# Performance work log

Measured on AMD Instinct MI355X. Metric: run time of the kernel, lower is better.

## Reference

```python
import jax, jax.numpy as jnp
import numpy as np

DIM = 256
HEADS = 8
HEAD_DIM = DIM // HEADS
SCALE = HEAD_DIM ** -0.5
WD, WH, WW = 2, 7, 7
N = WD * WH * WW            # 98 tokens per window
NW = 256                    # windows per sample
B = 2048                    # batch * num_windows
PBT_LEN = (2 * WD - 1) * (2 * WH - 1) * (2 * WW - 1)  # 507


def _relative_position_index():
    # Deterministic buffer from __init__: [N, N] int indices into pbt rows.
    coords = np.stack(np.meshgrid(np.arange(WD), np.arange(WH), np.arange(WW), indexing='ij'))
    coords = coords.reshape(3, -1)                      # [3, N]
    rel = coords[:, :, None] - coords[:, None, :]       # [3, N, N]
    rel = rel.transpose(1, 2, 0).copy()                 # [N, N, 3]
    rel[..., 0] += WD - 1
    rel[..., 1] += WH - 1
    rel[..., 2] += WW - 1
    rel[..., 0] *= (2 * WH - 1) * (2 * WW - 1)
    rel[..., 1] *= 2 * WW - 1
    return rel.sum(-1)                                  # [N, N]


def setup_inputs() -> dict:
    key = jax.random.key(0)
    ks = jax.random.split(key, 6)
    x = jax.random.normal(ks[0], (B, N, DIM), dtype=jnp.float32)
    mask = jax.random.normal(ks[1], (NW, N, N), dtype=jnp.float32)
    pbt = jax.random.normal(ks[2], (PBT_LEN, HEADS), dtype=jnp.float32) * 0.02
    qkv_w = jax.random.normal(ks[3], (3 * DIM, DIM), dtype=jnp.float32) * 0.02
    proj_w = jax.random.normal(ks[4], (DIM, DIM), dtype=jnp.float32) * 0.02
    proj_b = jax.random.normal(ks[5], (DIM,), dtype=jnp.float32) * 0.02
    rpi = jnp.asarray(_relative_position_index(), dtype=jnp.int32)
    return {"x": x, "mask": mask, "pbt": pbt, "qkv_w": qkv_w,
            "proj_w": proj_w, "proj_b": proj_b, "rpi": rpi}


def reference(x, mask, pbt, qkv_w, proj_w, proj_b, rpi):
    b, n, c = x.shape
    qkv = x @ qkv_w.T                                   # [b, n, 3c] (qkv_bias=False)
    q, k, v = jnp.split(qkv, 3, axis=-1)
    to_heads = lambda t: t.reshape(b, n, HEADS, HEAD_DIM).transpose(0, 2, 1, 3)
    q, k, v = to_heads(q), to_heads(k), to_heads(v)     # [b, h, n, d]

    attn = SCALE * jnp.einsum('bhnd,bhmd->bhnm', q, k)  # [b, h, n, n]
    # gathered relative-position bias: pbt[rpi] -> [n, n, h] -> [h, n, n]
    bias = pbt[rpi.reshape(-1)].reshape(n, n, HEADS).transpose(2, 0, 1)
    attn = attn + bias[None]

    n_w = mask.shape[0]
    attn = attn.reshape(b // n_w, n_w, HEADS, n, n) + mask[None, :, None]
    attn = attn.reshape(b, HEADS, n, n)

    attn = jax.nn.softmax(attn, axis=-1)
    out = jnp.einsum('bhnm,bhmd->bhnd', attn, v)        # [b, h, n, d]
    out = out.transpose(0, 2, 1, 3).reshape(b, n, c)
    return out @ proj_w.T + proj_b
```

## Files before the change

kernel.cpp:

```cpp
#include <hip/hip_runtime.h>
#include <hip/hip_bf16.h>
#include <math.h>

typedef float f32x4 __attribute__((ext_vector_type(4)));
typedef __bf16 bf16x8 __attribute__((ext_vector_type(8)));

#define NTOK 98
#define NWIN 2048
#define NN (NTOK * NTOK)
#define SCALE 0.17677669529663689f
#define MROWS (NWIN * NTOK)
#define PSTRIDE 9408

__device__ __forceinline__ void g2l16(const void* g, void* l) {
  typedef __attribute__((address_space(1))) const unsigned int GU;
  typedef __attribute__((address_space(3))) unsigned int LU;
  __builtin_amdgcn_global_load_lds((GU*)g, (LU*)l, 16, 0, 0);
}

__global__ void prep_kernel(const float* __restrict__ qkv_w, const float* __restrict__ proj_w,
                            const float* __restrict__ pbt, const int* __restrict__ rpi,
                            const float* __restrict__ mask,
                            __bf16* __restrict__ qkvw_b, __bf16* __restrict__ projw_b,
                            float* __restrict__ cmb) {
  int i = blockIdx.x * 256 + threadIdx.x;
  if (i < 768 * 256) qkvw_b[i] = (__bf16)qkv_w[i];
  if (i < 256 * 256) projw_b[i] = (__bf16)proj_w[i];
  if (i < 256 * 8 * NTOK * 128) {
    int mh = i / (NTOK * 128);
    int rem = i - mh * (NTOK * 128);
    int row = rem >> 7, j = rem & 127;
    if (j < NTOK) {
      int m = mh >> 3, h = mh & 7;
      cmb[i] = pbt[rpi[row * NTOK + j] * 8 + h] + mask[m * NN + row * NTOK + j];
    } else {
      cmb[i] = 0.f;
    }
  }
}

__launch_bounds__(256)
__global__ void gemm_qkv(const float* __restrict__ A, const __bf16* __restrict__ W,
                         __bf16* __restrict__ C) {
  __shared__ __align__(16) char As[65536];
  __shared__ __align__(16) char Bs[2][8192];
  const int m0 = blockIdx.x * 128;
  const int tid = threadIdx.x;
  const int lane = tid & 63;
  const int wid = tid >> 6;
  const int wm = wid & 1, wn = wid >> 1;
  const int lr = lane & 15;
  const int lg = lane >> 4;

  for (int c = tid; c < 128 * 32; c += 256) {
    int row = c >> 5, slot = c & 31;
    const float* ap = A + (size_t)(m0 + row) * 256 + slot * 8;
    float4 f0 = *(const float4*)ap;
    float4 f1 = *(const float4*)(ap + 4);
    bf16x8 hv;
    hv[0] = (__bf16)f0.x; hv[1] = (__bf16)f0.y; hv[2] = (__bf16)f0.z; hv[3] = (__bf16)f0.w;
    hv[4] = (__bf16)f1.x; hv[5] = (__bf16)f1.y; hv[6] = (__bf16)f1.z; hv[7] = (__bf16)f1.w;
    *(bf16x8*)(As + row * 512 + ((slot * 16) ^ ((row & 7) << 4))) = hv;
  }
  __syncthreads();

  for (int nt = 0; nt < 6; ++nt) {
    const int n0 = nt * 128;
    f32x4 acc[4][4] = {};

#pragma unroll
    for (int it2 = 0; it2 < 2; ++it2) {
      int wc = wid * 2 + it2;
      int cc = wc * 64 + lane;
      int row = cc >> 2, slot = cc & 3;
      int sw = (row & 3) ^ ((row >> 3) & 3);
      g2l16(W + (size_t)(n0 + row) * 256 + ((slot ^ sw) * 8), (void*)(Bs[0] + wc * 1024));
    }
    __syncthreads();

    for (int ks = 0; ks < 8; ++ks) {
      const int cur = ks & 1;
      if (ks < 7) {
#pragma unroll
        for (int it2 = 0; it2 < 2; ++it2) {
          int wc = wid * 2 + it2;
          int cc = wc * 64 + lane;
          int row = cc >> 2, slot = cc & 3;
          int sw = (row & 3) ^ ((row >> 3) & 3);
          g2l16(W + (size_t)(n0 + row) * 256 + (ks + 1) * 32 + ((slot ^ sw) * 8),
                (void*)(Bs[cur ^ 1] + wc * 1024));
        }
      }
      bf16x8 a[4], b[4];
#pragma unroll
      for (int m = 0; m < 4; ++m) {
        int row = wm * 64 + m * 16 + lr;
        a[m] = *(const bf16x8*)(As + row * 512 + ((ks * 64 + lg * 16) ^ ((row & 7) << 4)));
      }
#pragma unroll
      for (int n = 0; n < 4; ++n) {
        int row = wn * 64 + n * 16 + lr;
        int sw = (row & 3) ^ ((row >> 3) & 3);
        b[n] = *(const bf16x8*)(Bs[cur] + row * 64 + ((lg * 16) ^ (sw << 4)));
      }
#pragma unroll
      for (int m = 0; m < 4; ++m)
#pragma unroll
        for (int n = 0; n < 4; ++n)
          acc[m][n] = __builtin_amdgcn_mfma_f32_16x16x32_bf16(a[m], b[n], acc[m][n], 0, 0, 0);
      __syncthreads();
    }

#pragma unroll
    for (int m = 0; m < 4; ++m)
#pragma unroll
      for (int r = 0; r < 4; ++r) {
        unsigned row = m0 + wm * 64 + m * 16 + lg * 4 + r;
        unsigned win = row / NTOK;
        unsigned tok = row - win * NTOK;
#pragma unroll
        for (int n = 0; n < 4; ++n) {
          int col = n0 + wn * 64 + n * 16 + lr;
          int sec = col >> 8, dd = col & 255;
          int h = dd >> 5, d = dd & 31;
          C[(size_t)(win * 8 + h) * PSTRIDE + (size_t)sec * 3136 + tok * 32 + d] =
              (__bf16)acc[m][n][r];
        }
      }
  }
}

__launch_bounds__(128)
__global__ void attn_kernel(const __bf16* __restrict__ qkv, const float* __restrict__ cmb,
                            __bf16* __restrict__ y) {
  __shared__ __align__(16) char VTB[8192];
  int bx = blockIdx.x;
  int lb = (bx & 7) * 2048 + (bx >> 3);
  const int win = lb >> 3, h = lb & 7;
  const int tid = threadIdx.x;
  const int lane = tid & 63, wv = tid >> 6;
  const int lr = lane & 15, lg = lane >> 4;
  const f32x4 fz = {0.f, 0.f, 0.f, 0.f};

  const __bf16* qw = qkv + (size_t)(win * 8 + h) * PSTRIDE;
  const __bf16* kw = qw + 3136;
  const __bf16* vw = qw + 6272;
  const float* cw = cmb + (size_t)((win & 255) * 8 + h) * (NTOK * 128);

  for (int c = tid; c < 512; c += 128) {
    int j = c & 127; int jc = j < NTOK ? j : NTOK - 1;
    int d8 = (c >> 7) << 3;
    bf16x8 vv = *(const bf16x8*)(vw + jc * 32 + d8);
#pragma unroll
    for (int e = 0; e < 8; ++e) {
      int d = d8 + e;
      *(__bf16*)(VTB + d * 256 + ((2 * j) ^ ((d & 7) << 4))) = vv[e];
    }
  }

  bf16x8 bk[7];
#pragma unroll
  for (int jt = 0; jt < 7; ++jt) {
    int brow = ((jt >> 1) << 5) + ((lr >> 2) << 3) + ((jt & 1) << 2) + (lr & 3);
    int browc = brow < NTOK ? brow : NTOK - 1;
    bk[jt] = *(const bf16x8*)(kw + browc * 32 + lg * 8);
  }
  __syncthreads();

  for (int it = wv; it < 7; it += 2) {
    const int i0 = it * 16;
    const int qrow = i0 + lr;
    const int qrowc = qrow < NTOK ? qrow : NTOK - 1;
    bf16x8 aq = *(const bf16x8*)(qw + qrowc * 32 + lg * 8);

    const float* cr = cw + qrowc * 128;
    float4 cv[7];
#pragma unroll
    for (int jt = 0; jt < 7; ++jt) {
      int kb = ((jt >> 1) << 5) + lg * 8 + ((jt & 1) << 2);
      cv[jt] = *(const float4*)(cr + kb);
    }

    f32x4 s[7];
#pragma unroll
    for (int jt = 0; jt < 7; ++jt)
      s[jt] = __builtin_amdgcn_mfma_f32_16x16x32_bf16(bk[jt], aq, fz, 0, 0, 0);

    float sv[7][4];
    float mx = -INFINITY;
#pragma unroll
    for (int jt = 0; jt < 7; ++jt) {
      int kb = ((jt >> 1) << 5) + lg * 8 + ((jt & 1) << 2);
#pragma unroll
      for (int r = 0; r < 4; ++r) {
        float xv = (kb + r < NTOK) ? fmaf(SCALE, s[jt][r], (&cv[jt].x)[r]) : -INFINITY;
        sv[jt][r] = xv;
        mx = fmaxf(mx, xv);
      }
    }
    mx = fmaxf(mx, __shfl_xor(mx, 16));
    mx = fmaxf(mx, __shfl_xor(mx, 32));
    float sum = 0.f;
#pragma unroll
    for (int jt = 0; jt < 7; ++jt)
#pragma unroll
      for (int r = 0; r < 4; ++r) {
        float p = __expf(sv[jt][r] - mx);
        sv[jt][r] = p;
        sum += p;
      }
    sum += __shfl_xor(sum, 16);
    sum += __shfl_xor(sum, 32);
    const float rinv = 1.f / sum;

    bf16x8 pa[4];
#pragma unroll
    for (int ks = 0; ks < 4; ++ks)
#pragma unroll
      for (int e = 0; e < 8; ++e) {
        int jt = 2 * ks + (e >> 2);
        pa[ks][e] = (jt < 7) ? (__bf16)sv[jt][e & 3] : (__bf16)0.f;
      }

    float rv[4];
#pragma unroll
    for (int r = 0; r < 4; ++r) rv[r] = __shfl(rinv, lg * 4 + r);

#pragma unroll
    for (int dt = 0; dt < 2; ++dt) {
      f32x4 o = fz;
#pragma unroll
      for (int ks = 0; ks < 4; ++ks) {
        int vrow = dt * 16 + lr;
        bf16x8 vb = *(const bf16x8*)(VTB + vrow * 256 + ((ks * 64 + lg * 16) ^ ((vrow & 7) << 4)));
        o = __builtin_amdgcn_mfma_f32_16x16x32_bf16(pa[ks], vb, o, 0, 0, 0);
      }
#pragma unroll
      for (int r = 0; r < 4; ++r) {
        int row = i0 + lg * 4 + r;
        if (row < NTOK)
          y[((size_t)win * NTOK + row) * 256 + h * 32 + dt * 16 + lr] = (__bf16)(o[r] * rv[r]);
      }
    }
  }
}

__launch_bounds__(256)
__global__ void gemm_proj(const __bf16* __restrict__ A, const __bf16* __restrict__ W,
                          const float* __restrict__ pb, float* __restrict__ C) {
  __shared__ __align__(16) char As[65536];
  __shared__ __align__(16) char Bs[2][8192];
  const int m0 = blockIdx.x * 128;
  const int tid = threadIdx.x;
  const int lane = tid & 63;
  const int wid = tid >> 6;
  const int wm = wid & 1, wn = wid >> 1;
  const int lr = lane & 15;
  const int lg = lane >> 4;

#pragma unroll
  for (int it = 0; it < 16; ++it) {
    int c = wid * 16 + it;
    int cc = c * 64 + lane;
    int row = cc >> 5, slot = cc & 31;
    int src = slot ^ (row & 7);
    g2l16(A + (size_t)(m0 + row) * 256 + src * 8, (void*)(As + c * 1024));
  }
  __syncthreads();

  for (int nt = 0; nt < 2; ++nt) {
    const int n0 = nt * 128;
    f32x4 acc[4][4] = {};

#pragma unroll
    for (int it2 = 0; it2 < 2; ++it2) {
      int wc = wid * 2 + it2;
      int cc = wc * 64 + lane;
      int row = cc >> 2, slot = cc & 3;
      int sw = (row & 3) ^ ((row >> 3) & 3);
      g2l16(W + (size_t)(n0 + row) * 256 + ((slot ^ sw) * 8), (void*)(Bs[0] + wc * 1024));
    }
    __syncthreads();

    for (int ks = 0; ks < 8; ++ks) {
      const int cur = ks & 1;
      if (ks < 7) {
#pragma unroll
        for (int it2 = 0; it2 < 2; ++it2) {
          int wc = wid * 2 + it2;
          int cc = wc * 64 + lane;
          int row = cc >> 2, slot = cc & 3;
          int sw = (row & 3) ^ ((row >> 3) & 3);
          g2l16(W + (size_t)(n0 + row) * 256 + (ks + 1) * 32 + ((slot ^ sw) * 8),
                (void*)(Bs[cur ^ 1] + wc * 1024));
        }
      }
      bf16x8 a[4], b[4];
#pragma unroll
      for (int m = 0; m < 4; ++m) {
        int row = wm * 64 + m * 16 + lr;
        a[m] = *(const bf16x8*)(As + row * 512 + ((ks * 64 + lg * 16) ^ ((row & 7) << 4)));
      }
#pragma unroll
      for (int n = 0; n < 4; ++n) {
        int row = wn * 64 + n * 16 + lr;
        int sw = (row & 3) ^ ((row >> 3) & 3);
        b[n] = *(const bf16x8*)(Bs[cur] + row * 64 + ((lg * 16) ^ (sw << 4)));
      }
#pragma unroll
      for (int m = 0; m < 4; ++m)
#pragma unroll
        for (int n = 0; n < 4; ++n)
          acc[m][n] = __builtin_amdgcn_mfma_f32_16x16x32_bf16(a[m], b[n], acc[m][n], 0, 0, 0);
      __syncthreads();
    }

#pragma unroll
    for (int m = 0; m < 4; ++m) {
      int row = m0 + wm * 64 + m * 16 + lg * 4;
#pragma unroll
      for (int n = 0; n < 4; ++n) {
        int col = n0 + wn * 64 + n * 16 + lr;
        float bv = pb[col];
#pragma unroll
        for (int r = 0; r < 4; ++r)
          C[(size_t)(row + r) * 256 + col] = acc[m][n][r] + bv;
      }
    }
  }
}

extern "C" void kernel_launch(void* const* d_in, const int* in_sizes, int n_in,
                              void* d_out, int out_size, void* d_ws, size_t ws_size,
                              hipStream_t stream) {
  const float* x      = (const float*)d_in[0];
  const float* mask   = (const float*)d_in[1];
  const float* pbt    = (const float*)d_in[2];
  const float* qkv_w  = (const float*)d_in[3];
  const float* proj_w = (const float*)d_in[4];
  const float* proj_b = (const float*)d_in[5];
  const int*   rpi    = (const int*)d_in[6];
  float* out = (float*)d_out;

  char* ws = (char*)d_ws;
  __bf16* qkv      = (__bf16*)(ws);
  __bf16* y        = (__bf16*)(ws + 308281344);
  __bf16* qkvw_b   = (__bf16*)(ws + 411041792);
  __bf16* projw_b  = (__bf16*)(ws + 411435008);
  float*  cmb      = (float*) (ws + 411566080);

  int prep_n = 256 * 8 * NTOK * 128;
  prep_kernel<<<(prep_n + 255) / 256, 256, 0, stream>>>(qkv_w, proj_w, pbt, rpi, mask,
                                                        qkvw_b, projw_b, cmb);
  gemm_qkv<<<MROWS / 128, 256, 0, stream>>>(x, qkvw_b, qkv);
  attn_kernel<<<NWIN * 8, 128, 0, stream>>>(qkv, cmb, y);
  gemm_proj<<<MROWS / 128, 256, 0, stream>>>(y, projw_b, proj_b, out);
}
```

Baseline: 506.3 us.

## Retile QKV GEMM to 112-row blocks with triple-buffered weight prefetch

Changes the QKV projection GEMM to process 112-row M tiles (MROWS divisible by 112) with each wave owning all 7 M sub-tiles and a 32-column N slice. It replaces the double-buffered weight staging with a three-stage buffer that prefetches two K-steps ahead, using explicit vmcnt waits and raw barriers instead of __syncthreads. The goal is to hide global load latency and cut per-step synchronization. The trade-off is more LDS and registers and a different grid size, and the hand-written waitcnt logic could be fragile.

```diff
diff --git a/kernel.cpp b/kernel.cpp
--- a/kernel.cpp
+++ b/kernel.cpp
@@ -42,17 +42,17 @@
 __launch_bounds__(256)
 __global__ void gemm_qkv(const float* __restrict__ A, const __bf16* __restrict__ W,
                          __bf16* __restrict__ C) {
-  __shared__ __align__(16) char As[65536];
-  __shared__ __align__(16) char Bs[2][8192];
-  const int m0 = blockIdx.x * 128;
+  __shared__ __align__(16) char As[57344];
+  __shared__ __align__(16) char Bs[3][8192];
+  const int m0 = blockIdx.x * 112;
   const int tid = threadIdx.x;
   const int lane = tid & 63;
   const int wid = tid >> 6;
-  const int wm = wid & 1, wn = wid >> 1;
+  const int wn = wid;
   const int lr = lane & 15;
   const int lg = lane >> 4;
 
-  for (int c = tid; c < 128 * 32; c += 256) {
+  for (int c = tid; c < 112 * 32; c += 256) {
     int row = c >> 5, slot = c & 31;
     const float* ap = A + (size_t)(m0 + row) * 256 + slot * 8;
     float4 f0 = *(const float4*)ap;
@@ -66,61 +66,69 @@
 
   for (int nt = 0; nt < 6; ++nt) {
     const int n0 = nt * 128;
-    f32x4 acc[4][4] = {};
-
-#pragma unroll
-    for (int it2 = 0; it2 < 2; ++it2) {
-      int wc = wid * 2 + it2;
-      int cc = wc * 64 + lane;
-      int row = cc >> 2, slot = cc & 3;
-      int sw = (row & 3) ^ ((row >> 3) & 3);
-      g2l16(W + (size_t)(n0 + row) * 256 + ((slot ^ sw) * 8), (void*)(Bs[0] + wc * 1024));
-    }
-    __syncthreads();
+    f32x4 acc[7][2] = {};
+
+#pragma unroll
+    for (int st = 0; st < 2; ++st) {
+#pragma unroll
+      for (int it2 = 0; it2 < 2; ++it2) {
+        int wc = wid * 2 + it2;
+        int cc = wc * 64 + lane;
+        int row = cc >> 2, slot = cc & 3;
+        int sw = (row & 3) ^ ((row >> 3) & 3);
+        g2l16(W + (size_t)(n0 + row) * 256 + st * 32 + ((slot ^ sw) * 8),
+              (void*)(Bs[st] + wc * 1024));
+      }
+    }
+    asm volatile("s_waitcnt vmcnt(2)" ::: "memory");
+    __builtin_amdgcn_s_barrier();
+    __builtin_amdgcn_sched_barrier(0);
 
     for (int ks = 0; ks < 8; ++ks) {
-      const int cur = ks & 1;
-      if (ks < 7) {
+      const int cur = ks % 3;
+      if (ks < 6) {
+        const int nb = (ks + 2) % 3;
 #pragma unroll
         for (int it2 = 0; it2 < 2; ++it2) {
           int wc = wid * 2 + it2;
           int cc = wc * 64 + lane;
           int row = cc >> 2, slot = cc & 3;
           int sw = (row & 3) ^ ((row >> 3) & 3);
-          g2l16(W + (size_t)(n0 + row) * 256 + (ks + 1) * 32 + ((slot ^ sw) * 8),
-                (void*)(Bs[cur ^ 1] + wc * 1024));
+          g2l16(W + (size_t)(n0 + row) * 256 + (ks + 2) * 32 + ((slot ^ sw) * 8),
+                (void*)(Bs[nb] + wc * 1024));
         }
       }
-      bf16x8 a[4], b[4];
-#pragma unroll
-      for (int m = 0; m < 4; ++m) {
-        int row = wm * 64 + m * 16 + lr;
-        a[m] = *(const bf16x8*)(As + row * 512 + ((ks * 64 + lg * 16) ^ ((row & 7) << 4)));
-      }
-#pragma unroll
-      for (int n = 0; n < 4; ++n) {
-        int row = wn * 64 + n * 16 + lr;
+      bf16x8 b[2];
+#pragma unroll
+      for (int n = 0; n < 2; ++n) {
+        int row = wn * 32 + n * 16 + lr;
         int sw = (row & 3) ^ ((row >> 3) & 3);
         b[n] = *(const bf16x8*)(Bs[cur] + row * 64 + ((lg * 16) ^ (sw << 4)));
       }
 #pragma unroll
-      for (int m = 0; m < 4; ++m)
-#pragma unroll
-        for (int n = 0; n < 4; ++n)
-          acc[m][n] = __builtin_amdgcn_mfma_f32_16x16x32_bf16(a[m], b[n], acc[m][n], 0, 0, 0);
-      __syncthreads();
-    }
-
-#pragma unroll
-    for (int m = 0; m < 4; ++m)
+      for (int m = 0; m < 7; ++m) {
+        int row = m * 16 + lr;
+        bf16x8 a = *(const bf16x8*)(As + row * 512 + ((ks * 64 + lg * 16) ^ ((row & 7) << 4)));
+#pragma unroll
+        for (int n = 0; n < 2; ++n)
+          acc[m][n] = __builtin_amdgcn_mfma_f32_16x16x32_bf16(a, b[n], acc[m][n], 0, 0, 0);
+      }
+      if (ks < 6)      asm volatile("s_waitcnt vmcnt(2)" ::: "memory");
+      else             asm volatile("s_waitcnt vmcnt(0)" ::: "memory");
+      __builtin_amdgcn_s_barrier();
+      __builtin_amdgcn_sched_barrier(0);
+    }
+
+#pragma unroll
+    for (int m = 0; m < 7; ++m)
 #pragma unroll
       for (int r = 0; r < 4; ++r) {
-        unsigned row = m0 + wm * 64 + m * 16 + lg * 4 + r;
+        unsigned row = m0 + m * 16 + lg * 4 + r;
         unsigned win = row / NTOK;
         unsigned tok = row - win * NTOK;
 #pragma unroll
-        for (int n = 0; n < 4; ++n) {
-          int col = n0 + wn * 64 + n * 16 + lr;
+        for (int n = 0; n < 2; ++n) {
+          int col = n0 + wn * 32 + n * 16 + lr;
           int sec = col >> 8, dd = col & 255;
           int h = dd >> 5, d = dd & 31;
           C[(size_t)(win * 8 + h) * PSTRIDE + (size_t)sec * 3136 + tok * 32 + d] =
@@ -352,7 +360,7 @@
   int prep_n = 256 * 8 * NTOK * 128;
   prep_kernel<<<(prep_n + 255) / 256, 256, 0, stream>>>(qkv_w, proj_w, pbt, rpi, mask,
                                                         qkvw_b, projw_b, cmb);
-  gemm_qkv<<<MROWS / 128, 256, 0, stream>>>(x, qkvw_b, qkv);
+  gemm_qkv<<<MROWS / 112, 256, 0, stream>>>(x, qkvw_b, qkv);
   attn_kernel<<<NWIN * 8, 128, 0, stream>>>(qkv, cmb, y);
   gemm_proj<<<MROWS / 128, 256, 0, stream>>>(y, projw_b, proj_b, out);
 }
```

After: 504.6 us. About the same (-0.3%).

## Vectorize prep kernel and load QKV weights directly into registers

Applied to the files above, without the earlier changes.

The prep kernel now handles four output elements per thread, with vectorized weight conversion and float4 stores of the combined bias-plus-mask table, which cuts the thread count fourfold. The QKV GEMM drops its double-buffered LDS staging of the weight tile. Each wave instead loads its B fragments straight from global memory into registers, prefetching one k-step ahead, which removes the per-step barriers and LDS traffic. The cost is redundant global (L2) reads of the weights across the two M-waves, and the weight-load latency is exposed if the one-step prefetch cannot hide it.

```diff
diff --git a/kernel.cpp b/kernel.cpp
--- a/kernel.cpp
+++ b/kernel.cpp
@@ -23,19 +23,40 @@
                             const float* __restrict__ mask,
                             __bf16* __restrict__ qkvw_b, __bf16* __restrict__ projw_b,
                             float* __restrict__ cmb) {
-  int i = blockIdx.x * 256 + threadIdx.x;
-  if (i < 768 * 256) qkvw_b[i] = (__bf16)qkv_w[i];
-  if (i < 256 * 256) projw_b[i] = (__bf16)proj_w[i];
-  if (i < 256 * 8 * NTOK * 128) {
-    int mh = i / (NTOK * 128);
-    int rem = i - mh * (NTOK * 128);
-    int row = rem >> 7, j = rem & 127;
+  int i4 = blockIdx.x * 256 + threadIdx.x;
+  if (i4 < 768 * 256 / 8) {
+    const float* p = qkv_w + (size_t)i4 * 8;
+    float4 f0 = *(const float4*)p;
+    float4 f1 = *(const float4*)(p + 4);
+    bf16x8 hv;
+    hv[0] = (__bf16)f0.x; hv[1] = (__bf16)f0.y; hv[2] = (__bf16)f0.z; hv[3] = (__bf16)f0.w;
+    hv[4] = (__bf16)f1.x; hv[5] = (__bf16)f1.y; hv[6] = (__bf16)f1.z; hv[7] = (__bf16)f1.w;
+    *(bf16x8*)(qkvw_b + (size_t)i4 * 8) = hv;
+  }
+  if (i4 < 256 * 256 / 8) {
+    const float* p = proj_w + (size_t)i4 * 8;
+    float4 f0 = *(const float4*)p;
+    float4 f1 = *(const float4*)(p + 4);
+    bf16x8 hv;
+    hv[0] = (__bf16)f0.x; hv[1] = (__bf16)f0.y; hv[2] = (__bf16)f0.z; hv[3] = (__bf16)f0.w;
+    hv[4] = (__bf16)f1.x; hv[5] = (__bf16)f1.y; hv[6] = (__bf16)f1.z; hv[7] = (__bf16)f1.w;
+    *(bf16x8*)(projw_b + (size_t)i4 * 8) = hv;
+  }
+  if (i4 < 256 * 8 * NTOK * 32) {
+    int mh = i4 / (NTOK * 32);
+    int rem = i4 - mh * (NTOK * 32);
+    int row = rem >> 5, j4 = rem & 31;
+    int j = j4 * 4;
+    int m = mh >> 3, h = mh & 7;
+    float4 v = {0.f, 0.f, 0.f, 0.f};
     if (j < NTOK) {
-      int m = mh >> 3, h = mh & 7;
-      cmb[i] = pbt[rpi[row * NTOK + j] * 8 + h] + mask[m * NN + row * NTOK + j];
-    } else {
-      cmb[i] = 0.f;
-    }
+      const float* mrow = mask + (size_t)m * NN + row * NTOK;
+      const int* rrow = rpi + row * NTOK;
+#pragma unroll
+      for (int c = 0; c < 4; ++c)
+        if (j + c < NTOK) (&v.x)[c] = pbt[rrow[j + c] * 8 + h] + mrow[j + c];
+    }
+    *(float4*)(cmb + (size_t)(mh * NTOK + row) * 128 + j) = v;
   }
 }
 
@@ -43,7 +64,6 @@
 __global__ void gemm_qkv(const float* __restrict__ A, const __bf16* __restrict__ W,
                          __bf16* __restrict__ C) {
   __shared__ __align__(16) char As[65536];
-  __shared__ __align__(16) char Bs[2][8192];
   const int m0 = blockIdx.x * 128;
   const int tid = threadIdx.x;
   const int lane = tid & 63;
@@ -68,47 +88,35 @@
     const int n0 = nt * 128;
     f32x4 acc[4][4] = {};
 
-#pragma unroll
-    for (int it2 = 0; it2 < 2; ++it2) {
-      int wc = wid * 2 + it2;
-      int cc = wc * 64 + lane;
-      int row = cc >> 2, slot = cc & 3;
-      int sw = (row & 3) ^ ((row >> 3) & 3);
-      g2l16(W + (size_t)(n0 + row) * 256 + ((slot ^ sw) * 8), (void*)(Bs[0] + wc * 1024));
-    }
-    __syncthreads();
-
+    bf16x8 bcur[4];
+#pragma unroll
+    for (int n = 0; n < 4; ++n)
+      bcur[n] = *(const bf16x8*)(W + (size_t)(n0 + wn * 64 + n * 16 + lr) * 256 + lg * 8);
+
+#pragma unroll
     for (int ks = 0; ks < 8; ++ks) {
-      const int cur = ks & 1;
+      bf16x8 bnext[4];
       if (ks < 7) {
 #pragma unroll
-        for (int it2 = 0; it2 < 2; ++it2) {
-          int wc = wid * 2 + it2;
-          int cc = wc * 64 + lane;
-          int row = cc >> 2, slot = cc & 3;
-          int sw = (row & 3) ^ ((row >> 3) & 3);
-          g2l16(W + (size_t)(n0 + row) * 256 + (ks + 1) * 32 + ((slot ^ sw) * 8),
-                (void*)(Bs[cur ^ 1] + wc * 1024));
-        }
-      }
-      bf16x8 a[4], b[4];
+        for (int n = 0; n < 4; ++n)
+          bnext[n] = *(const bf16x8*)(W + (size_t)(n0 + wn * 64 + n * 16 + lr) * 256 +
+                                      (ks + 1) * 32 + lg * 8);
+      }
+      bf16x8 a[4];
 #pragma unroll
       for (int m = 0; m < 4; ++m) {
         int row = wm * 64 + m * 16 + lr;
         a[m] = *(const bf16x8*)(As + row * 512 + ((ks * 64 + lg * 16) ^ ((row & 7) << 4)));
       }
 #pragma unroll
-      for (int n = 0; n < 4; ++n) {
-        int row = wn * 64 + n * 16 + lr;
-        int sw = (row & 3) ^ ((row >> 3) & 3);
-        b[n] = *(const bf16x8*)(Bs[cur] + row * 64 + ((lg * 16) ^ (sw << 4)));
-      }
-#pragma unroll
       for (int m = 0; m < 4; ++m)
 #pragma unroll
         for (int n = 0; n < 4; ++n)
-          acc[m][n] = __builtin_amdgcn_mfma_f32_16x16x32_bf16(a[m], b[n], acc[m][n], 0, 0, 0);
-      __syncthreads();
+          acc[m][n] = __builtin_amdgcn_mfma_f32_16x16x32_bf16(a[m], bcur[n], acc[m][n], 0, 0, 0);
+      if (ks < 7) {
+#pragma unroll
+        for (int n = 0; n < 4; ++n) bcur[n] = bnext[n];
+      }
     }
 
 #pragma unroll
@@ -349,7 +357,7 @@
   __bf16* projw_b  = (__bf16*)(ws + 411435008);
   float*  cmb      = (float*) (ws + 411566080);
 
-  int prep_n = 256 * 8 * NTOK * 128;
+  int prep_n = 256 * 8 * NTOK * 32;
   prep_kernel<<<(prep_n + 255) / 256, 256, 0, stream>>>(qkv_w, proj_w, pbt, rpi, mask,
                                                         qkvw_b, projw_b, cmb);
   gemm_qkv<<<MROWS / 128, 256, 0, stream>>>(x, qkvw_b, qkv);
```

After: 591.7 us. 16.9% more time.
